# Kernel optimization log

Measured on AMD Instinct MI355X. Metric: run time of the kernel, lower is better.

## Reference

```python
import jax, jax.numpy as jnp
import numpy as np

V, E, NNZ = 50000, 25000, 200000
F_IN, HID, D = 128, 256, 4
H1, C = 16, 40  # h = [256, 16, 40] per the code's width schedule for l=2


def setup_inputs() -> dict:
    key = jax.random.key(0)
    ks = jax.random.split(key, 16)
    inp = {
        'x': jax.random.normal(ks[0], (V, F_IN), jnp.float32),
        'eattr': jax.random.normal(ks[1], (E, F_IN), jnp.float32),  # init_hedge='rand'
        'node_idx': jax.random.randint(ks[2], (NNZ,), 0, V),
        'edge_idx': jax.random.randint(ks[3], (NNZ,), 0, E),
        # lin: F_IN -> D*HID (shared for nodes and hyperedge attrs)
        'Wlin': jax.random.normal(ks[4], (F_IN, D * HID), jnp.float32) / np.sqrt(F_IN),
        'blin': jnp.zeros((D * HID,), jnp.float32),
        # diag sheaf builder: per-incidence, per-head restriction-map scalar
        'w1': jax.random.normal(ks[5], (HID, D), jnp.float32) / np.sqrt(HID),
        'w2': jax.random.normal(ks[6], (HID, D), jnp.float32) / np.sqrt(HID),
        'bs': jnp.zeros((D,), jnp.float32),
        # hypergraph conv layers
        'W0': jax.random.normal(ks[7], (HID, H1), jnp.float32) / np.sqrt(HID),
        'b0': jnp.zeros((H1,), jnp.float32),
        'W1': jax.random.normal(ks[8], (H1, C), jnp.float32) / np.sqrt(H1),
        'b1': jnp.zeros((C,), jnp.float32),
        # lin2: h[-1]*d -> num_classes, no bias
        'W2': jax.random.normal(ks[9], (D * C, C), jnp.float32) / np.sqrt(D * C),
    }
    return inp


def reference(x, eattr, node_idx, edge_idx, Wlin, blin, w1, w2, bs, W0, b0, W1, b1, W2):
    # lift node / hyperedge features into d stalks: [V, d, HID], [E, d, HID]
    Hn = (x @ Wlin + blin).reshape(V, D, HID)
    He = (eattr @ Wlin + blin).reshape(E, D, HID)

    # diagonal sheaf restriction maps, one scalar per (incidence, head)
    hv = Hn[node_idx]                      # [NNZ, D, HID] gather
    he = He[edge_idx]                      # [NNZ, D, HID] gather
    s = jnp.tanh(jnp.einsum('ndh,hd->nd', hv, w1)
                 + jnp.einsum('ndh,hd->nd', he, w2) + bs)   # [NNZ, D]

    # degree normalization (degree_norm): D^{-1}, inf -> 0
    deg_e = jax.ops.segment_sum(jnp.ones((NNZ,), jnp.float32), edge_idx, num_segments=E)
    inv_e = jnp.where(deg_e > 0, 1.0 / deg_e, 0.0)
    deg_v = jax.ops.segment_sum(jnp.ones((NNZ,), jnp.float32), node_idx, num_segments=V)
    inv_v = jnp.where(deg_v > 0, 1.0 / deg_v, 0.0)

    def apply_L(Hf):  # sheaf Laplacian L = I - D^{-1} F^T B F : [V, D, c] -> [V, D, c]
        m = jax.ops.segment_sum(s[:, :, None] * Hf[node_idx], edge_idx, num_segments=E)
        m = m * inv_e[:, None, None]       # hyperedge aggregation [E, D, c]
        a = jax.ops.segment_sum(s[:, :, None] * m[edge_idx], node_idx, num_segments=V)
        a = a * inv_v[:, None, None]       # back-scatter to nodes [V, D, c]
        return Hf - a

    H = jax.nn.relu(apply_L(Hn) @ W0 + b0)   # [V, D, 16]
    H = jax.nn.relu(apply_L(H) @ W1 + b1)    # [V, D, 40]
    return H.reshape(V, D * C) @ W2          # [V, 40]
```

## Files before the change

kernel.cpp:

```cpp
#include <hip/hip_runtime.h>
#include <hip/hip_fp16.h>
#include <stdint.h>

#define V_N 50000
#define E_N 25000
#define NNZ_N 200000
#define CHUNK 2048

__global__ __launch_bounds__(256) void k_zero(int* __restrict__ p, int n) {
  int i = blockIdx.x * 256 + threadIdx.x;
  if (i < n) p[i] = 0;
}

__global__ __launch_bounds__(64) void k_fuse(
    const float* __restrict__ Wlin, const float* __restrict__ blin,
    const float* __restrict__ w1, const float* __restrict__ w2,
    const float* __restrict__ bs, const float* __restrict__ W0,
    const float* __restrict__ b0,
    float* __restrict__ Wf0, float* __restrict__ u1, float* __restrict__ u2,
    float* __restrict__ cb, float* __restrict__ bf0, float* __restrict__ sbias)
{
  __shared__ float row[1024];
  int f = blockIdx.x;
  for (int t = threadIdx.x; t < 1024; t += 64) row[t] = Wlin[f * 1024 + t];
  __syncthreads();
  int j = threadIdx.x;
  int d = j >> 4, jj = j & 15;
  float acc = 0.f;
  for (int h = 0; h < 256; ++h) acc += row[d * 256 + h] * W0[h * 16 + jj];
  Wf0[f * 64 + j] = acc;
  if (j < 4) {
    float a1 = 0.f, a2 = 0.f;
    for (int h = 0; h < 256; ++h) {
      a1 += row[j * 256 + h] * w1[h * 4 + j];
      a2 += row[j * 256 + h] * w2[h * 4 + j];
    }
    u1[f * 4 + j] = a1;
    u2[f * 4 + j] = a2;
  }
  if (f == 0) {
    float ab = 0.f;
    for (int h = 0; h < 256; ++h) ab += blin[d * 256 + h] * W0[h * 16 + jj];
    cb[j] = ab;
    bf0[j] = b0[jj];
    if (j < 4) {
      float sb = bs[j];
      for (int h = 0; h < 256; ++h) sb += blin[j * 256 + h] * (w1[h * 4 + j] + w2[h * 4 + j]);
      sbias[j] = sb;
    }
  }
}

__global__ __launch_bounds__(256) void k_degrees(
    const int* __restrict__ node_idx, const int* __restrict__ edge_idx,
    int* __restrict__ degE, int* __restrict__ degV)
{
  int i = blockIdx.x * 256 + threadIdx.x;
  if (i < NNZ_N) {
    atomicAdd(&degE[edge_idx[i]], 1);
    atomicAdd(&degV[node_idx[i]], 1);
  }
}

__global__ __launch_bounds__(256) void k_scanA(
    const int* __restrict__ degE, const int* __restrict__ degV,
    int* __restrict__ offE, int* __restrict__ offV,
    int* __restrict__ bsumE, int* __restrict__ bsumV, int nchunkE)
{
  bool isE = (int)blockIdx.x < nchunkE;
  const int* deg = isE ? degE : degV;
  int* off = isE ? offE : offV;
  int* bsum = isE ? bsumE : bsumV;
  int n = isE ? E_N : V_N;
  int chunk = isE ? blockIdx.x : (blockIdx.x - nchunkE);
  int base = chunk * CHUNK;
  int tid = threadIdx.x;
  int vals[8];
  int tsum = 0;
  for (int it = 0; it < 8; ++it) {
    int idx = base + tid * 8 + it;
    int v = (idx < n) ? deg[idx] : 0;
    vals[it] = tsum;
    tsum += v;
  }
  __shared__ int sA[256], sB[256];
  sA[tid] = tsum;
  __syncthreads();
  int* src = sA; int* dst = sB;
  for (int sh = 1; sh < 256; sh <<= 1) {
    dst[tid] = src[tid] + (tid >= sh ? src[tid - sh] : 0);
    __syncthreads();
    int* t = src; src = dst; dst = t;
  }
  int excl = src[tid] - tsum;
  for (int it = 0; it < 8; ++it) {
    int idx = base + tid * 8 + it;
    if (idx < n) off[idx] = excl + vals[it];
  }
  if (tid == 255) bsum[chunk] = src[255];
}

__global__ __launch_bounds__(64) void k_scanB(
    int* __restrict__ bsumE, int* __restrict__ bsumV, int nchunkE, int nchunkV)
{
  if (threadIdx.x == 0) {
    int* b = (blockIdx.x == 0) ? bsumE : bsumV;
    int n = (blockIdx.x == 0) ? nchunkE : nchunkV;
    int run = 0;
    for (int i = 0; i < n; ++i) { int v = b[i]; b[i] = run; run += v; }
  }
}

__global__ __launch_bounds__(256) void k_scanC_inv(
    int* __restrict__ offE, int* __restrict__ offV,
    const int* __restrict__ bsumE, const int* __restrict__ bsumV,
    const int* __restrict__ degE, const int* __restrict__ degV,
    float* __restrict__ invE, float* __restrict__ invV, int nchunkE)
{
  bool isE = (int)blockIdx.x < nchunkE;
  int* off = isE ? offE : offV;
  const int* bsum = isE ? bsumE : bsumV;
  const int* deg = isE ? degE : degV;
  float* inv = isE ? invE : invV;
  int n = isE ? E_N : V_N;
  int chunk = isE ? blockIdx.x : (blockIdx.x - nchunkE);
  int base = chunk * CHUNK;
  int add = bsum[chunk];
  for (int it = 0; it < 8; ++it) {
    int idx = base + threadIdx.x * 8 + it;
    if (idx < n) {
      off[idx] += add;
      int dg = deg[idx];
      inv[idx] = dg > 0 ? 1.0f / (float)dg : 0.0f;
    }
  }
}

__global__ __launch_bounds__(256) void k_gemm_node(
    const float* __restrict__ x, const float* __restrict__ Wf0,
    const float* __restrict__ u1, const float* __restrict__ cb,
    __half* __restrict__ G0h, float* __restrict__ svx)
{
  __shared__ float Xt[64 * 132];
  __shared__ float us[512];
  int tid = threadIdx.x;
  int row0 = blockIdx.x * 64;
  #pragma unroll
  for (int it = 0; it < 8; ++it) {
    int fi = it * 1024 + tid * 4;
    int r = fi >> 7, c = fi & 127;
    float4 val = make_float4(0.f, 0.f, 0.f, 0.f);
    int gr = row0 + r;
    if (gr < V_N) val = *(const float4*)(x + (size_t)gr * 128 + c);
    *(float4*)&Xt[r * 132 + c] = val;
  }
  for (int k2 = tid; k2 < 512; k2 += 256) us[k2] = u1[k2];
  int ty = tid >> 4, tx = tid & 15;
  float4 cbr = *(const float4*)(cb + tx * 4);
  __syncthreads();

  float acc[4][4];
  #pragma unroll
  for (int i = 0; i < 4; ++i) {
    acc[i][0] = cbr.x; acc[i][1] = cbr.y; acc[i][2] = cbr.z; acc[i][3] = cbr.w;
  }
  #pragma unroll 2
  for (int k0 = 0; k0 < 128; k0 += 4) {
    float A_[4][4], W_[4][4];
    #pragma unroll
    for (int kk = 0; kk < 4; ++kk)
      *(float4*)&W_[kk][0] = *(const float4*)(Wf0 + (size_t)(k0 + kk) * 64 + tx * 4);
    #pragma unroll
    for (int i = 0; i < 4; ++i)
      *(float4*)&A_[i][0] = *(const float4*)&Xt[(ty * 4 + i) * 132 + k0];
    #pragma unroll
    for (int i = 0; i < 4; ++i)
      #pragma unroll
      for (int kk = 0; kk < 4; ++kk)
        #pragma unroll
        for (int j = 0; j < 4; ++j)
          acc[i][j] += A_[i][kk] * W_[kk][j];
  }
  #pragma unroll
  for (int i = 0; i < 4; ++i) {
    int gr = row0 + ty * 4 + i;
    if (gr < V_N) {
      __half2* dst = (__half2*)(G0h + (size_t)gr * 64 + tx * 4);
      dst[0] = __floats2half2_rn(acc[i][0], acc[i][1]);
      dst[1] = __floats2half2_rn(acc[i][2], acc[i][3]);
    }
  }
  int rs = tid >> 2, dS = tid & 3;
  float a2 = 0.f;
  for (int k = 0; k < 128; ++k)
    a2 += Xt[rs * 132 + k] * us[k * 4 + dS];
  int gr = row0 + rs;
  if (gr < V_N) svx[gr * 4 + dS] = a2;
}

__global__ __launch_bounds__(256) void k_gemm_edge(
    const float* __restrict__ eattr, const float* __restrict__ u2,
    float* __restrict__ sex)
{
  __shared__ float Xt[64 * 132];
  __shared__ float us[512];
  int tid = threadIdx.x;
  int row0 = blockIdx.x * 64;
  #pragma unroll
  for (int it = 0; it < 8; ++it) {
    int fi = it * 1024 + tid * 4;
    int r = fi >> 7, c = fi & 127;
    float4 val = make_float4(0.f, 0.f, 0.f, 0.f);
    int gr = row0 + r;
    if (gr < E_N) val = *(const float4*)(eattr + (size_t)gr * 128 + c);
    *(float4*)&Xt[r * 132 + c] = val;
  }
  for (int k2 = tid; k2 < 512; k2 += 256) us[k2] = u2[k2];
  __syncthreads();
  int rs = tid >> 2, dS = tid & 3;
  float a2 = 0.f;
  for (int k = 0; k < 128; ++k)
    a2 += Xt[rs * 132 + k] * us[k * 4 + dS];
  int gr = row0 + rs;
  if (gr < E_N) sex[gr * 4 + dS] = a2;
}

__global__ __launch_bounds__(256) void k_fill_s(
    const int* __restrict__ node_idx, const int* __restrict__ edge_idx,
    const int* __restrict__ offE, const int* __restrict__ offV,
    int* __restrict__ curE, int* __restrict__ curV,
    int* __restrict__ csrEv, int* __restrict__ csrVe,
    float* __restrict__ sE4, float* __restrict__ sV4,
    const float* __restrict__ svx, const float* __restrict__ sex,
    const float* __restrict__ sbias,
    const float* __restrict__ invE, const float* __restrict__ invV)
{
  int i = blockIdx.x * 256 + threadIdx.x;
  if (i >= NNZ_N) return;
  int v = node_idx[i], e = edge_idx[i];
  float4 a = *(const float4*)(svx + (size_t)v * 4);
  float4 b = *(const float4*)(sex + (size_t)e * 4);
  float4 sb = *(const float4*)(sbias);
  float4 r;
  r.x = tanhf(a.x + b.x + sb.x);
  r.y = tanhf(a.y + b.y + sb.y);
  r.z = tanhf(a.z + b.z + sb.z);
  r.w = tanhf(a.w + b.w + sb.w);
  float ie = invE[e], iv = invV[v];
  int pe = atomicAdd(&curE[e], 1);
  int slotE = offE[e] + pe;
  csrEv[slotE] = v;
  float4 re = make_float4(r.x * ie, r.y * ie, r.z * ie, r.w * ie);
  *(float4*)(sE4 + (size_t)slotE * 4) = re;
  int pv = atomicAdd(&curV[v], 1);
  int slotV = offV[v] + pv;
  csrVe[slotV] = e;
  float4 rv = make_float4(r.x * iv, r.y * iv, r.z * iv, r.w * iv);
  *(float4*)(sV4 + (size_t)slotV * 4) = rv;
}

__global__ __launch_bounds__(256) void k_eagg(
    const __half* __restrict__ Hin, const int* __restrict__ csrEv,
    const float* __restrict__ sE4,
    const int* __restrict__ offE, const int* __restrict__ degE,
    __half* __restrict__ m)
{
  int g = threadIdx.x >> 6, lane = threadIdx.x & 63;
  int e = blockIdx.x * 4 + g;
  if (e >= E_N) return;
  int o0 = offE[e], dg = degE[e];
  int dsh = (lane >> 4) & 3;
  float acc = 0.f;
  for (int base = 0; base < dg; base += 16) {
    int idx = base + (lane & 15);
    int vv = (idx < dg) ? csrEv[o0 + idx] : 0;
    int sidx = base * 4 + lane;
    float ss = (sidx < dg * 4) ? sE4[(size_t)o0 * 4 + sidx] : 0.f;
    int lim = min(16, dg - base);
    #pragma unroll 4
    for (int t = 0; t < lim; ++t) {
      int v = __shfl(vv, t);
      float sv = __shfl(ss, t * 4 + dsh);
      acc += sv * __half2float(Hin[(size_t)v * 64 + lane]);
    }
  }
  m[(size_t)e * 64 + lane] = __float2half(acc);
}

__global__ __launch_bounds__(256) void k_nagg(
    const __half* __restrict__ base_, const __half* __restrict__ m,
    const int* __restrict__ csrVe, const float* __restrict__ sV4,
    const int* __restrict__ offV, const int* __restrict__ degV,
    const float* __restrict__ bf0, int doRelu,
    __half* __restrict__ outH, float* __restrict__ outF)
{
  int g = threadIdx.x >> 6, lane = threadIdx.x & 63;
  int v = blockIdx.x * 4 + g;
  if (v >= V_N) return;
  int o0 = offV[v], dg = degV[v];
  int dsh = (lane >> 4) & 3;
  float acc = 0.f;
  for (int base = 0; base < dg; base += 16) {
    int idx = base + (lane & 15);
    int ee = (idx < dg) ? csrVe[o0 + idx] : 0;
    int sidx = base * 4 + lane;
    float ss = (sidx < dg * 4) ? sV4[(size_t)o0 * 4 + sidx] : 0.f;
    int lim = min(16, dg - base);
    #pragma unroll 4
    for (int t = 0; t < lim; ++t) {
      int e = __shfl(ee, t);
      float sv = __shfl(ss, t * 4 + dsh);
      acc += sv * __half2float(m[(size_t)e * 64 + lane]);
    }
  }
  float r = __half2float(base_[(size_t)v * 64 + lane]) - acc;
  if (doRelu) {
    r = fmaxf(r + bf0[lane], 0.f);
    outH[(size_t)v * 64 + lane] = __float2half(r);
  } else {
    outF[(size_t)v * 64 + lane] = r;
  }
}

__global__ __launch_bounds__(256) void k_final(
    const float* __restrict__ A, const float* __restrict__ W1, const float* __restrict__ b1,
    const float* __restrict__ W2, float* __restrict__ out)
{
  __shared__ float W2s[160 * 40];
  __shared__ float t[32 * 164];
  __shared__ float W1s[640];
  __shared__ float b1s[40];
  int tid = threadIdx.x;
  int v0 = blockIdx.x * 32;

  for (int k = tid; k < 1600; k += 256) ((float4*)W2s)[k] = ((const float4*)W2)[k];
  for (int k = tid; k < 640; k += 256) W1s[k] = W1[k];
  if (tid < 40) b1s[tid] = b1[tid];
  __syncthreads();

  if (tid < 160) {
    int rg = tid / 20, cg = tid % 20;
    int r0 = rg * 4;
    int j0 = cg * 8;
    int d = cg / 5;
    int jloc = j0 - d * 40;
    float a[4][16];
    #pragma unroll
    for (int i = 0; i < 4; ++i) {
      int gr = v0 + r0 + i;
      #pragma unroll
      for (int c4 = 0; c4 < 4; ++c4) {
        float4 val = make_float4(0.f, 0.f, 0.f, 0.f);
        if (gr < V_N) val = *(const float4*)(A + (size_t)gr * 64 + d * 16 + c4 * 4);
        *(float4*)&a[i][c4 * 4] = val;
      }
    }
    float acc1[4][8];
    #pragma unroll
    for (int i = 0; i < 4; ++i)
      #pragma unroll
      for (int jj = 0; jj < 8; ++jj) acc1[i][jj] = b1s[jloc + jj];
    #pragma unroll
    for (int c = 0; c < 16; ++c) {
      float w[8];
      *(float4*)&w[0] = *(const float4*)&W1s[c * 40 + jloc];
      *(float4*)&w[4] = *(const float4*)&W1s[c * 40 + jloc + 4];
      #pragma unroll
      for (int i = 0; i < 4; ++i)
        #pragma unroll
        for (int jj = 0; jj < 8; ++jj)
          acc1[i][jj] += a[i][c] * w[jj];
    }
    #pragma unroll
    for (int i = 0; i < 4; ++i) {
      float4 lo = make_float4(fmaxf(acc1[i][0], 0.f), fmaxf(acc1[i][1], 0.f),
                              fmaxf(acc1[i][2], 0.f), fmaxf(acc1[i][3], 0.f));
      float4 hi = make_float4(fmaxf(acc1[i][4], 0.f), fmaxf(acc1[i][5], 0.f),
                              fmaxf(acc1[i][6], 0.f), fmaxf(acc1[i][7], 0.f));
      *(float4*)&t[(r0 + i) * 164 + j0] = lo;
      *(float4*)&t[(r0 + i) * 164 + j0 + 4] = hi;
    }
  }
  __syncthreads();

  if (tid < 160) {
    int rg2 = tid / 10, cg2 = tid % 10;
    float acc2[2][4] = {{0.f, 0.f, 0.f, 0.f}, {0.f, 0.f, 0.f, 0.f}};
    for (int k0 = 0; k0 < 160; k0 += 4) {
      float a0[4], a1[4], w[4][4];
      *(float4*)a0 = *(const float4*)&t[(rg2 * 2 + 0) * 164 + k0];
      *(float4*)a1 = *(const float4*)&t[(rg2 * 2 + 1) * 164 + k0];
      #pragma unroll
      for (int kk = 0; kk < 4; ++kk)
        *(float4*)&w[kk][0] = *(const float4*)&W2s[(k0 + kk) * 40 + cg2 * 4];
      #pragma unroll
      for (int kk = 0; kk < 4; ++kk)
        #pragma unroll
        for (int j = 0; j < 4; ++j) {
          acc2[0][j] += a0[kk] * w[kk][j];
          acc2[1][j] += a1[kk] * w[kk][j];
        }
    }
    #pragma unroll
    for (int i = 0; i < 2; ++i) {
      int gr = v0 + rg2 * 2 + i;
      if (gr < V_N)
        *(float4*)(out + (size_t)gr * 40 + cg2 * 4) =
            make_float4(acc2[i][0], acc2[i][1], acc2[i][2], acc2[i][3]);
    }
  }
}

extern "C" void kernel_launch(void* const* d_in, const int* in_sizes, int n_in,
                              void* d_out, int out_size, void* d_ws, size_t ws_size,
                              hipStream_t stream) {
  (void)in_sizes; (void)n_in; (void)out_size; (void)ws_size;
  const float* x = (const float*)d_in[0];
  const float* eattr = (const float*)d_in[1];
  const int* node_idx = (const int*)d_in[2];
  const int* edge_idx = (const int*)d_in[3];
  const float* Wlin = (const float*)d_in[4];
  const float* blin = (const float*)d_in[5];
  const float* w1 = (const float*)d_in[6];
  const float* w2 = (const float*)d_in[7];
  const float* bs = (const float*)d_in[8];
  const float* W0 = (const float*)d_in[9];
  const float* b0 = (const float*)d_in[10];
  const float* W1 = (const float*)d_in[11];
  const float* b1 = (const float*)d_in[12];
  const float* W2 = (const float*)d_in[13];
  float* out = (float*)d_out;

  char* p = (char*)d_ws;
  auto alloc = [&](size_t bytes) { char* q = p; p += (bytes + 255) & ~(size_t)255; return q; };
  float*  Wf0   = (float*)alloc(8192 * 4);
  float*  u1    = (float*)alloc(512 * 4);
  float*  u2    = (float*)alloc(512 * 4);
  float*  cbv   = (float*)alloc(64 * 4);
  float*  bf0   = (float*)alloc(64 * 4);
  float*  sbias = (float*)alloc(4 * 4);
  __half* G0h   = (__half*)alloc((size_t)V_N * 64 * 2);
  __half* Hbh   = (__half*)alloc((size_t)V_N * 64 * 2);
  __half* mbh   = (__half*)alloc((size_t)E_N * 64 * 2);
  float*  Af    = (float*)alloc((size_t)V_N * 64 * 4);
  float*  svx   = (float*)alloc((size_t)V_N * 4 * 4);
  float*  sex   = (float*)alloc((size_t)E_N * 4 * 4);
  float*  sE4   = (float*)alloc((size_t)NNZ_N * 4 * 4);
  float*  sV4   = (float*)alloc((size_t)NNZ_N * 4 * 4);
  float*  invE  = (float*)alloc(E_N * 4);
  float*  invV  = (float*)alloc(V_N * 4);
  int* zeroRegion = (int*)alloc((size_t)(2 * E_N + 2 * V_N) * 4);
  int* degE = zeroRegion;
  int* degV = degE + E_N;
  int* curE = degV + V_N;
  int* curV = curE + E_N;
  int* offE  = (int*)alloc(E_N * 4);
  int* offV  = (int*)alloc(V_N * 4);
  int* csrEv = (int*)alloc((size_t)NNZ_N * 4);
  int* csrVe = (int*)alloc((size_t)NNZ_N * 4);
  int* bsumE = (int*)alloc(64 * 4);
  int* bsumV = (int*)alloc(64 * 4);

  int nZero = 2 * E_N + 2 * V_N;
  int nchunkE = (E_N + CHUNK - 1) / CHUNK;
  int nchunkV = (V_N + CHUNK - 1) / CHUNK;
  int nbNode = (V_N + 63) / 64;
  int nbEdge = (E_N + 63) / 64;

  hipLaunchKernelGGL(k_zero, dim3((nZero + 255) / 256), dim3(256), 0, stream, zeroRegion, nZero);
  hipLaunchKernelGGL(k_fuse, dim3(128), dim3(64), 0, stream,
                     Wlin, blin, w1, w2, bs, W0, b0, Wf0, u1, u2, cbv, bf0, sbias);
  hipLaunchKernelGGL(k_degrees, dim3((NNZ_N + 255) / 256), dim3(256), 0, stream,
                     node_idx, edge_idx, degE, degV);
  hipLaunchKernelGGL(k_scanA, dim3(nchunkE + nchunkV), dim3(256), 0, stream,
                     degE, degV, offE, offV, bsumE, bsumV, nchunkE);
  hipLaunchKernelGGL(k_scanB, dim3(2), dim3(64), 0, stream, bsumE, bsumV, nchunkE, nchunkV);
  hipLaunchKernelGGL(k_scanC_inv, dim3(nchunkE + nchunkV), dim3(256), 0, stream,
                     offE, offV, bsumE, bsumV, degE, degV, invE, invV, nchunkE);
  hipLaunchKernelGGL(k_gemm_node, dim3(nbNode), dim3(256), 0, stream,
                     x, Wf0, u1, cbv, G0h, svx);
  hipLaunchKernelGGL(k_gemm_edge, dim3(nbEdge), dim3(256), 0, stream,
                     eattr, u2, sex);
  hipLaunchKernelGGL(k_fill_s, dim3((NNZ_N + 255) / 256), dim3(256), 0, stream,
                     node_idx, edge_idx, offE, offV, curE, curV, csrEv, csrVe,
                     sE4, sV4, svx, sex, sbias, invE, invV);
  hipLaunchKernelGGL(k_eagg, dim3((E_N + 3) / 4), dim3(256), 0, stream,
                     G0h, csrEv, sE4, offE, degE, mbh);
  hipLaunchKernelGGL(k_nagg, dim3((V_N + 3) / 4), dim3(256), 0, stream,
                     G0h, mbh, csrVe, sV4, offV, degV, bf0, 1, Hbh, (float*)nullptr);
  hipLaunchKernelGGL(k_eagg, dim3((E_N + 3) / 4), dim3(256), 0, stream,
                     Hbh, csrEv, sE4, offE, degE, mbh);
  hipLaunchKernelGGL(k_nagg, dim3((V_N + 3) / 4), dim3(256), 0, stream,
                     Hbh, mbh, csrVe, sV4, offV, degV, bf0, 0, (__half*)nullptr, Af);
  hipLaunchKernelGGL(k_final, dim3((V_N + 31) / 32), dim3(256), 0, stream, Af, W1, b1, W2, out);
}
```

Baseline: 325.0 us.

## Vectorize gather-aggregation over 4 neighbors per wave and parallelize chunk-sum scan

The edge and node aggregation kernels now split each 64-lane wave into four 16-lane groups. Each group processes a different neighbor and loads 4 halves per lane with 8-byte loads, and the partial sums are combined by xor shuffles. The goal is more memory-level parallelism and fewer, wider gather loads per neighbor, at the cost of extra shuffle reductions and idle lanes when the degree is not a multiple of 4. The serial single-thread block-sum scan becomes a 64-lane shuffle scan, which assumes the chunk count is at most 64, and W0 is staged in shared memory in the fuse kernel.

```diff
diff --git a/kernel.cpp b/kernel.cpp
--- a/kernel.cpp
+++ b/kernel.cpp
@@ -21,13 +21,15 @@
     float* __restrict__ cb, float* __restrict__ bf0, float* __restrict__ sbias)
 {
   __shared__ float row[1024];
+  __shared__ float W0s[4096];
   int f = blockIdx.x;
   for (int t = threadIdx.x; t < 1024; t += 64) row[t] = Wlin[f * 1024 + t];
+  for (int t = threadIdx.x; t < 4096; t += 64) W0s[t] = W0[t];
   __syncthreads();
   int j = threadIdx.x;
   int d = j >> 4, jj = j & 15;
   float acc = 0.f;
-  for (int h = 0; h < 256; ++h) acc += row[d * 256 + h] * W0[h * 16 + jj];
+  for (int h = 0; h < 256; ++h) acc += row[d * 256 + h] * W0s[h * 16 + jj];
   Wf0[f * 64 + j] = acc;
   if (j < 4) {
     float a1 = 0.f, a2 = 0.f;
@@ -40,7 +42,7 @@
   }
   if (f == 0) {
     float ab = 0.f;
-    for (int h = 0; h < 256; ++h) ab += blin[d * 256 + h] * W0[h * 16 + jj];
+    for (int h = 0; h < 256; ++h) ab += blin[d * 256 + h] * W0s[h * 16 + jj];
     cb[j] = ab;
     bf0[j] = b0[jj];
     if (j < 4) {
@@ -103,12 +105,16 @@
 __global__ __launch_bounds__(64) void k_scanB(
     int* __restrict__ bsumE, int* __restrict__ bsumV, int nchunkE, int nchunkV)
 {
-  if (threadIdx.x == 0) {
-    int* b = (blockIdx.x == 0) ? bsumE : bsumV;
-    int n = (blockIdx.x == 0) ? nchunkE : nchunkV;
-    int run = 0;
-    for (int i = 0; i < n; ++i) { int v = b[i]; b[i] = run; run += v; }
-  }
+  int* b = (blockIdx.x == 0) ? bsumE : bsumV;
+  int n = (blockIdx.x == 0) ? nchunkE : nchunkV;
+  int tid = threadIdx.x;
+  int v = (tid < n) ? b[tid] : 0;
+  int s = v;
+  for (int sh = 1; sh < 64; sh <<= 1) {
+    int o = __shfl_up(s, sh);
+    if (tid >= sh) s += o;
+  }
+  if (tid < n) b[tid] = s - v;
 }
 
 __global__ __launch_bounds__(256) void k_scanC_inv(
@@ -269,22 +275,40 @@
   int e = blockIdx.x * 4 + g;
   if (e >= E_N) return;
   int o0 = offE[e], dg = degE[e];
-  int dsh = (lane >> 4) & 3;
-  float acc = 0.f;
+  int qw = lane >> 4, L16 = lane & 15;
+  int d = L16 >> 2;
+  float4 acc = make_float4(0.f, 0.f, 0.f, 0.f);
   for (int base = 0; base < dg; base += 16) {
-    int idx = base + (lane & 15);
+    int idx = base + L16;
     int vv = (idx < dg) ? csrEv[o0 + idx] : 0;
     int sidx = base * 4 + lane;
     float ss = (sidx < dg * 4) ? sE4[(size_t)o0 * 4 + sidx] : 0.f;
     int lim = min(16, dg - base);
-    #pragma unroll 4
-    for (int t = 0; t < lim; ++t) {
-      int v = __shfl(vv, t);
-      float sv = __shfl(ss, t * 4 + dsh);
-      acc += sv * __half2float(Hin[(size_t)v * 64 + lane]);
-    }
-  }
-  m[(size_t)e * 64 + lane] = __float2half(acc);
+    #pragma unroll 2
+    for (int q = 0; q < lim; q += 4) {
+      int tloc = q + qw;
+      int v = __shfl(vv, tloc);
+      float sv = __shfl(ss, tloc * 4 + d);
+      if (tloc < lim) {
+        uint2 raw = *(const uint2*)(Hin + (size_t)v * 64 + L16 * 4);
+        __half2 ha = *reinterpret_cast<__half2*>(&raw.x);
+        __half2 hb = *reinterpret_cast<__half2*>(&raw.y);
+        float2 fa = __half22float2(ha), fb = __half22float2(hb);
+        acc.x += sv * fa.x; acc.y += sv * fa.y;
+        acc.z += sv * fb.x; acc.w += sv * fb.y;
+      }
+    }
+  }
+  acc.x += __shfl_xor(acc.x, 16); acc.y += __shfl_xor(acc.y, 16);
+  acc.z += __shfl_xor(acc.z, 16); acc.w += __shfl_xor(acc.w, 16);
+  acc.x += __shfl_xor(acc.x, 32); acc.y += __shfl_xor(acc.y, 32);
+  acc.z += __shfl_xor(acc.z, 32); acc.w += __shfl_xor(acc.w, 32);
+  if (qw == 0) {
+    __half2 oa = __floats2half2_rn(acc.x, acc.y);
+    __half2 ob = __floats2half2_rn(acc.z, acc.w);
+    uint2 o; o.x = *(unsigned int*)&oa; o.y = *(unsigned int*)&ob;
+    *(uint2*)(m + (size_t)e * 64 + L16 * 4) = o;
+  }
 }
 
 __global__ __launch_bounds__(256) void k_nagg(
@@ -298,27 +322,52 @@
   int v = blockIdx.x * 4 + g;
   if (v >= V_N) return;
   int o0 = offV[v], dg = degV[v];
-  int dsh = (lane >> 4) & 3;
-  float acc = 0.f;
+  int qw = lane >> 4, L16 = lane & 15;
+  int d = L16 >> 2;
+  float4 acc = make_float4(0.f, 0.f, 0.f, 0.f);
   for (int base = 0; base < dg; base += 16) {
-    int idx = base + (lane & 15);
+    int idx = base + L16;
     int ee = (idx < dg) ? csrVe[o0 + idx] : 0;
     int sidx = base * 4 + lane;
     float ss = (sidx < dg * 4) ? sV4[(size_t)o0 * 4 + sidx] : 0.f;
     int lim = min(16, dg - base);
-    #pragma unroll 4
-    for (int t = 0; t < lim; ++t) {
-      int e = __shfl(ee, t);
-      float sv = __shfl(ss, t * 4 + dsh);
-      acc += sv * __half2float(m[(size_t)e * 64 + lane]);
-    }
-  }
-  float r = __half2float(base_[(size_t)v * 64 + lane]) - acc;
-  if (doRelu) {
-    r = fmaxf(r + bf0[lane], 0.f);
-    outH[(size_t)v * 64 + lane] = __float2half(r);
-  } else {
-    outF[(size_t)v * 64 + lane] = r;
+    #pragma unroll 2
+    for (int q = 0; q < lim; q += 4) {
+      int tloc = q + qw;
+      int e = __shfl(ee, tloc);
+      float sv = __shfl(ss, tloc * 4 + d);
+      if (tloc < lim) {
+        uint2 raw = *(const uint2*)(m + (size_t)e * 64 + L16 * 4);
+        __half2 ha = *reinterpret_cast<__half2*>(&raw.x);
+        __half2 hb = *reinterpret_cast<__half2*>(&raw.y);
+        float2 fa = __half22float2(ha), fb = __half22float2(hb);
+        acc.x += sv * fa.x; acc.y += sv * fa.y;
+        acc.z += sv * fb.x; acc.w += sv * fb.y;
+      }
+    }
+  }
+  acc.x += __shfl_xor(acc.x, 16); acc.y += __shfl_xor(acc.y, 16);
+  acc.z += __shfl_xor(acc.z, 16); acc.w += __shfl_xor(acc.w, 16);
+  acc.x += __shfl_xor(acc.x, 32); acc.y += __shfl_xor(acc.y, 32);
+  acc.z += __shfl_xor(acc.z, 32); acc.w += __shfl_xor(acc.w, 32);
+  if (qw == 0) {
+    uint2 braw = *(const uint2*)(base_ + (size_t)v * 64 + L16 * 4);
+    __half2 b0h = *reinterpret_cast<__half2*>(&braw.x);
+    __half2 b1h = *reinterpret_cast<__half2*>(&braw.y);
+    float2 bfa = __half22float2(b0h), bfb = __half22float2(b1h);
+    float r0 = bfa.x - acc.x, r1 = bfa.y - acc.y;
+    float r2 = bfb.x - acc.z, r3 = bfb.y - acc.w;
+    if (doRelu) {
+      float4 bf = *(const float4*)(bf0 + L16 * 4);
+      r0 = fmaxf(r0 + bf.x, 0.f); r1 = fmaxf(r1 + bf.y, 0.f);
+      r2 = fmaxf(r2 + bf.z, 0.f); r3 = fmaxf(r3 + bf.w, 0.f);
+      __half2 oa = __floats2half2_rn(r0, r1);
+      __half2 ob = __floats2half2_rn(r2, r3);
+      uint2 o; o.x = *(unsigned int*)&oa; o.y = *(unsigned int*)&ob;
+      *(uint2*)(outH + (size_t)v * 64 + L16 * 4) = o;
+    } else {
+      *(float4*)(outF + (size_t)v * 64 + L16 * 4) = make_float4(r0, r1, r2, r3);
+    }
   }
 }
 
```

After: 293.4 us. -9.7%, faster.

## Vectorize sparse aggregation kernels with 8-wide half loads and multi-neighbour lanes

Applied to the files above, without the earlier changes.

The edge and node aggregation kernels now assign 8 lanes per neighbour row, each loading 8 halves as one uint4. A wave processes 8 incident nodes per iteration (half-wave per node, 4 at a time, for node aggregation), and partial sums are combined with xor shuffles. This replaces the serial per-neighbour loop with scalar half loads and should improve memory-level parallelism for degree around 4–8. It also replaces the serial single-thread block-sum scan with a wave shuffle scan and stages W0 in shared memory in the weight-fusion kernel. The new scan assumes at most 64 chunks.

```diff
diff --git a/kernel.cpp b/kernel.cpp
--- a/kernel.cpp
+++ b/kernel.cpp
@@ -21,13 +21,15 @@
     float* __restrict__ cb, float* __restrict__ bf0, float* __restrict__ sbias)
 {
   __shared__ float row[1024];
+  __shared__ float W0s[4096];
   int f = blockIdx.x;
   for (int t = threadIdx.x; t < 1024; t += 64) row[t] = Wlin[f * 1024 + t];
+  for (int t = threadIdx.x; t < 4096; t += 64) W0s[t] = W0[t];
   __syncthreads();
   int j = threadIdx.x;
   int d = j >> 4, jj = j & 15;
   float acc = 0.f;
-  for (int h = 0; h < 256; ++h) acc += row[d * 256 + h] * W0[h * 16 + jj];
+  for (int h = 0; h < 256; ++h) acc += row[d * 256 + h] * W0s[h * 16 + jj];
   Wf0[f * 64 + j] = acc;
   if (j < 4) {
     float a1 = 0.f, a2 = 0.f;
@@ -40,7 +42,7 @@
   }
   if (f == 0) {
     float ab = 0.f;
-    for (int h = 0; h < 256; ++h) ab += blin[d * 256 + h] * W0[h * 16 + jj];
+    for (int h = 0; h < 256; ++h) ab += blin[d * 256 + h] * W0s[h * 16 + jj];
     cb[j] = ab;
     bf0[j] = b0[jj];
     if (j < 4) {
@@ -103,12 +105,16 @@
 __global__ __launch_bounds__(64) void k_scanB(
     int* __restrict__ bsumE, int* __restrict__ bsumV, int nchunkE, int nchunkV)
 {
-  if (threadIdx.x == 0) {
-    int* b = (blockIdx.x == 0) ? bsumE : bsumV;
-    int n = (blockIdx.x == 0) ? nchunkE : nchunkV;
-    int run = 0;
-    for (int i = 0; i < n; ++i) { int v = b[i]; b[i] = run; run += v; }
-  }
+  int* b = (blockIdx.x == 0) ? bsumE : bsumV;
+  int n = (blockIdx.x == 0) ? nchunkE : nchunkV;
+  int tid = threadIdx.x;
+  int v = (tid < n) ? b[tid] : 0;
+  int s = v;
+  for (int sh = 1; sh < 64; sh <<= 1) {
+    int o = __shfl_up(s, sh);
+    if (tid >= sh) s += o;
+  }
+  if (tid < n) b[tid] = s - v;
 }
 
 __global__ __launch_bounds__(256) void k_scanC_inv(
@@ -265,26 +271,49 @@
     const int* __restrict__ offE, const int* __restrict__ degE,
     __half* __restrict__ m)
 {
-  int g = threadIdx.x >> 6, lane = threadIdx.x & 63;
-  int e = blockIdx.x * 4 + g;
+  int wave = threadIdx.x >> 6, lane = threadIdx.x & 63;
+  int e = blockIdx.x * 4 + wave;
   if (e >= E_N) return;
   int o0 = offE[e], dg = degE[e];
-  int dsh = (lane >> 4) & 3;
-  float acc = 0.f;
-  for (int base = 0; base < dg; base += 16) {
-    int idx = base + (lane & 15);
-    int vv = (idx < dg) ? csrEv[o0 + idx] : 0;
-    int sidx = base * 4 + lane;
-    float ss = (sidx < dg * 4) ? sE4[(size_t)o0 * 4 + sidx] : 0.f;
-    int lim = min(16, dg - base);
-    #pragma unroll 4
-    for (int t = 0; t < lim; ++t) {
-      int v = __shfl(vv, t);
-      float sv = __shfl(ss, t * 4 + dsh);
-      acc += sv * __half2float(Hin[(size_t)v * 64 + lane]);
-    }
-  }
-  m[(size_t)e * 64 + lane] = __float2half(acc);
+  int hw = lane >> 3, L8 = lane & 7;
+  int d = L8 >> 1;
+  float4 a0 = make_float4(0.f, 0.f, 0.f, 0.f);
+  float4 a1 = make_float4(0.f, 0.f, 0.f, 0.f);
+  for (int base = 0; base < dg; base += 8) {
+    int vv = 0;
+    if (lane < 8 && base + lane < dg) vv = csrEv[o0 + base + lane];
+    float ss = 0.f;
+    if (lane < 32 && base * 4 + lane < dg * 4) ss = sE4[(size_t)o0 * 4 + base * 4 + lane];
+    int tloc = base + hw;
+    int v = __shfl(vv, hw);
+    float sv = __shfl(ss, hw * 4 + d);
+    if (tloc < dg) {
+      uint4 raw = *(const uint4*)(Hin + (size_t)v * 64 + L8 * 8);
+      float2 f0 = __half22float2(*reinterpret_cast<__half2*>(&raw.x));
+      float2 f1 = __half22float2(*reinterpret_cast<__half2*>(&raw.y));
+      float2 f2 = __half22float2(*reinterpret_cast<__half2*>(&raw.z));
+      float2 f3 = __half22float2(*reinterpret_cast<__half2*>(&raw.w));
+      a0.x += sv * f0.x; a0.y += sv * f0.y; a0.z += sv * f1.x; a0.w += sv * f1.y;
+      a1.x += sv * f2.x; a1.y += sv * f2.y; a1.z += sv * f3.x; a1.w += sv * f3.y;
+    }
+  }
+  #pragma unroll
+  for (int off = 8; off <= 32; off <<= 1) {
+    a0.x += __shfl_xor(a0.x, off); a0.y += __shfl_xor(a0.y, off);
+    a0.z += __shfl_xor(a0.z, off); a0.w += __shfl_xor(a0.w, off);
+    a1.x += __shfl_xor(a1.x, off); a1.y += __shfl_xor(a1.y, off);
+    a1.z += __shfl_xor(a1.z, off); a1.w += __shfl_xor(a1.w, off);
+  }
+  if (hw == 0) {
+    __half2 o0h = __floats2half2_rn(a0.x, a0.y);
+    __half2 o1h = __floats2half2_rn(a0.z, a0.w);
+    __half2 o2h = __floats2half2_rn(a1.x, a1.y);
+    __half2 o3h = __floats2half2_rn(a1.z, a1.w);
+    uint4 o;
+    o.x = *(unsigned int*)&o0h; o.y = *(unsigned int*)&o1h;
+    o.z = *(unsigned int*)&o2h; o.w = *(unsigned int*)&o3h;
+    *(uint4*)(m + (size_t)e * 64 + L8 * 8) = o;
+  }
 }
 
 __global__ __launch_bounds__(256) void k_nagg(
@@ -294,31 +323,69 @@
     const float* __restrict__ bf0, int doRelu,
     __half* __restrict__ outH, float* __restrict__ outF)
 {
-  int g = threadIdx.x >> 6, lane = threadIdx.x & 63;
-  int v = blockIdx.x * 4 + g;
+  int half = threadIdx.x >> 5;
+  int v = blockIdx.x * 8 + half;
   if (v >= V_N) return;
+  int lane = threadIdx.x & 63;
+  int ll = lane & 31;
+  int s0 = lane & 32;
   int o0 = offV[v], dg = degV[v];
-  int dsh = (lane >> 4) & 3;
-  float acc = 0.f;
-  for (int base = 0; base < dg; base += 16) {
-    int idx = base + (lane & 15);
-    int ee = (idx < dg) ? csrVe[o0 + idx] : 0;
-    int sidx = base * 4 + lane;
-    float ss = (sidx < dg * 4) ? sV4[(size_t)o0 * 4 + sidx] : 0.f;
-    int lim = min(16, dg - base);
-    #pragma unroll 4
-    for (int t = 0; t < lim; ++t) {
-      int e = __shfl(ee, t);
-      float sv = __shfl(ss, t * 4 + dsh);
-      acc += sv * __half2float(m[(size_t)e * 64 + lane]);
-    }
-  }
-  float r = __half2float(base_[(size_t)v * 64 + lane]) - acc;
-  if (doRelu) {
-    r = fmaxf(r + bf0[lane], 0.f);
-    outH[(size_t)v * 64 + lane] = __float2half(r);
-  } else {
-    outF[(size_t)v * 64 + lane] = r;
+  int hw = ll >> 3, L8 = ll & 7;
+  int d = L8 >> 1;
+  float4 a0 = make_float4(0.f, 0.f, 0.f, 0.f);
+  float4 a1 = make_float4(0.f, 0.f, 0.f, 0.f);
+  for (int base = 0; base < dg; base += 4) {
+    int ee = 0;
+    if (ll < 4 && base + ll < dg) ee = csrVe[o0 + base + ll];
+    float ss = 0.f;
+    if (ll < 16 && base * 4 + ll < dg * 4) ss = sV4[(size_t)o0 * 4 + base * 4 + ll];
+    int tloc = base + hw;
+    int e = __shfl(ee, s0 + hw);
+    float sv = __shfl(ss, s0 + hw * 4 + d);
+    if (tloc < dg) {
+      uint4 raw = *(const uint4*)(m + (size_t)e * 64 + L8 * 8);
+      float2 f0 = __half22float2(*reinterpret_cast<__half2*>(&raw.x));
+      float2 f1 = __half22float2(*reinterpret_cast<__half2*>(&raw.y));
+      float2 f2 = __half22float2(*reinterpret_cast<__half2*>(&raw.z));
+      float2 f3 = __half22float2(*reinterpret_cast<__half2*>(&raw.w));
+      a0.x += sv * f0.x; a0.y += sv * f0.y; a0.z += sv * f1.x; a0.w += sv * f1.y;
+      a1.x += sv * f2.x; a1.y += sv * f2.y; a1.z += sv * f3.x; a1.w += sv * f3.y;
+    }
+  }
+  #pragma unroll
+  for (int off = 8; off <= 16; off <<= 1) {
+    a0.x += __shfl_xor(a0.x, off); a0.y += __shfl_xor(a0.y, off);
+    a0.z += __shfl_xor(a0.z, off); a0.w += __shfl_xor(a0.w, off);
+    a1.x += __shfl_xor(a1.x, off); a1.y += __shfl_xor(a1.y, off);
+    a1.z += __shfl_xor(a1.z, off); a1.w += __shfl_xor(a1.w, off);
+  }
+  if (hw == 0) {
+    uint4 braw = *(const uint4*)(base_ + (size_t)v * 64 + L8 * 8);
+    float2 b0f = __half22float2(*reinterpret_cast<__half2*>(&braw.x));
+    float2 b1f = __half22float2(*reinterpret_cast<__half2*>(&braw.y));
+    float2 b2f = __half22float2(*reinterpret_cast<__half2*>(&braw.z));
+    float2 b3f = __half22float2(*reinterpret_cast<__half2*>(&braw.w));
+    float r0 = b0f.x - a0.x, r1 = b0f.y - a0.y, r2 = b1f.x - a0.z, r3 = b1f.y - a0.w;
+    float r4 = b2f.x - a1.x, r5 = b2f.y - a1.y, r6 = b3f.x - a1.z, r7 = b3f.y - a1.w;
+    if (doRelu) {
+      float4 bfa = *(const float4*)(bf0 + L8 * 8);
+      float4 bfb = *(const float4*)(bf0 + L8 * 8 + 4);
+      r0 = fmaxf(r0 + bfa.x, 0.f); r1 = fmaxf(r1 + bfa.y, 0.f);
+      r2 = fmaxf(r2 + bfa.z, 0.f); r3 = fmaxf(r3 + bfa.w, 0.f);
+      r4 = fmaxf(r4 + bfb.x, 0.f); r5 = fmaxf(r5 + bfb.y, 0.f);
+      r6 = fmaxf(r6 + bfb.z, 0.f); r7 = fmaxf(r7 + bfb.w, 0.f);
+      __half2 o0h = __floats2half2_rn(r0, r1);
+      __half2 o1h = __floats2half2_rn(r2, r3);
+      __half2 o2h = __floats2half2_rn(r4, r5);
+      __half2 o3h = __floats2half2_rn(r6, r7);
+      uint4 o;
+      o.x = *(unsigned int*)&o0h; o.y = *(unsigned int*)&o1h;
+      o.z = *(unsigned int*)&o2h; o.w = *(unsigned int*)&o3h;
+      *(uint4*)(outH + (size_t)v * 64 + L8 * 8) = o;
+    } else {
+      *(float4*)(outF + (size_t)v * 64 + L8 * 8) = make_float4(r0, r1, r2, r3);
+      *(float4*)(outF + (size_t)v * 64 + L8 * 8 + 4) = make_float4(r4, r5, r6, r7);
+    }
   }
 }
 
@@ -486,11 +553,11 @@
                      sE4, sV4, svx, sex, sbias, invE, invV);
   hipLaunchKernelGGL(k_eagg, dim3((E_N + 3) / 4), dim3(256), 0, stream,
                      G0h, csrEv, sE4, offE, degE, mbh);
-  hipLaunchKernelGGL(k_nagg, dim3((V_N + 3) / 4), dim3(256), 0, stream,
+  hipLaunchKernelGGL(k_nagg, dim3((V_N + 7) / 8), dim3(256), 0, stream,
                      G0h, mbh, csrVe, sV4, offV, degV, bf0, 1, Hbh, (float*)nullptr);
   hipLaunchKernelGGL(k_eagg, dim3((E_N + 3) / 4), dim3(256), 0, stream,
                      Hbh, csrEv, sE4, offE, degE, mbh);
-  hipLaunchKernelGGL(k_nagg, dim3((V_N + 3) / 4), dim3(256), 0, stream,
+  hipLaunchKernelGGL(k_nagg, dim3((V_N + 7) / 8), dim3(256), 0, stream,
                      Hbh, mbh, csrVe, sV4, offV, degV, bf0, 0, (__half*)nullptr, Af);
   hipLaunchKernelGGL(k_final, dim3((V_N + 31) / 32), dim3(256), 0, stream, Af, W1, b1, W2, out);
 }
```

After: 284.1 us. 1.14x faster.
